# Kernel tuning notes

Hardware: AMD Instinct MI355X
Metric: run time of the kernel (lower is better)

The kernel has to match this reference:

```python
import jax, jax.numpy as jnp
import numpy as np
from math import comb

N_DERIV = 4          # num_derivatives
ODE_DIM = 512        # ode_dimension
K = ODE_DIM * (N_DERIV + 1)


def _build_system(n, d):
    # system_matrices_1d: A_1d = flip(pascal), Q_1d = flip(hilbert), chol(Q_1d)
    x = np.arange(n + 1)
    B = np.array([[comb(i, j) for j in range(n + 1)] for i in range(n + 1)], dtype=np.float64)
    A1 = B[::-1, ::-1]                                  # flip both axes
    Hil = 1.0 / (x[:, None] + x[None, :] + 1.0)
    Q1 = Hil[::-1, ::-1]
    L1 = np.linalg.cholesky(Q1)
    a = np.kron(np.eye(d), A1)
    q = np.kron(np.eye(d), L1)
    return jnp.asarray(a, jnp.float32), jnp.asarray(q, jnp.float32)


def _qr_r(x):
    # sqrtm_to_cholesky: upper-triangular factor from reduced QR
    return jnp.linalg.qr(x)[1]


def setup_inputs() -> dict:
    key = jax.random.key(0)
    k1, k2, k3, k4, k5 = jax.random.split(key, 5)
    a, q_sqrtm_lower = _build_system(N_DERIV, ODE_DIM)
    m0 = jax.random.normal(k1, (K,), dtype=jnp.float32)
    l0 = jnp.tril(jax.random.normal(k2, (K, K), dtype=jnp.float32) * 0.05)
    H = jax.random.normal(k3, (ODE_DIM, K), dtype=jnp.float32) * 0.1
    bias = jax.random.normal(k4, (ODE_DIM,), dtype=jnp.float32)
    dt = jax.random.uniform(k5, (1,), dtype=jnp.float32, minval=0.05, maxval=0.15)
    return {"m0": m0, "l0": l0, "H": H, "bias": bias, "dt": dt,
            "a": a, "q_sqrtm_lower": q_sqrtm_lower}


def reference(m0, l0, H, bias, dt, a, q_sqrtm_lower):
    d = H.shape[0]
    k = m0.shape[0]
    n1 = k // d                       # num_derivatives + 1
    # --- assemble_preconditioner ---
    powers = jnp.arange(n1 - 1, -1, -1, dtype=m0.dtype)
    scales = jnp.exp(jax.lax.lgamma(powers + 1.0))
    pw = powers + 0.5
    adt = jnp.abs(dt[0])
    p = jnp.tile(adt ** pw / scales, d)          # (k,)
    p_inv = jnp.tile(adt ** (-pw) * scales, d)   # (k,)
    # --- extrapolate_mean ---
    m0_p = p_inv * m0
    m_ext_p = a @ m0_p
    m_ext = p * m_ext_p
    # EK-style linearized observation residual
    m_obs = H @ m_ext - bias                     # (d,)
    # --- estimate_error ---
    l_obs_ns_e = H @ (p_inv[:, None] * q_sqrtm_lower)            # (d,k)
    l_obs_raw = _qr_r(l_obs_ns_e.T).T                            # lower (d,d)
    res_white = jax.scipy.linalg.solve_triangular(l_obs_raw.T, m_obs, lower=False)
    diffusion = jnp.sqrt(jnp.dot(res_white, res_white) / res_white.size)
    error = diffusion * jnp.sqrt(jnp.einsum('nj,nj->n', l_obs_raw, l_obs_raw))
    # --- complete_extrapolation (sum_of_sqrtm_factors) ---
    R1 = (a @ (p_inv[:, None] * l0)).T           # (k,k)
    R2 = (diffusion * q_sqrtm_lower).T           # (k,k)
    l_ext_p = _qr_r(jnp.vstack([R1, R2])).T      # lower (k,k)
    l_ext = p[:, None] * l_ext_p
    # --- final_correction ---
    l_obs_ns = H @ l_ext                         # (d,k)
    l_obs = _qr_r(l_obs_ns.T).T                  # lower (d,d)
    crosscov = l_ext @ l_obs_ns.T                # (k,d)
    gain = jax.scipy.linalg.cho_solve((l_obs, True), crosscov.T).T  # (k,d)
    m_cor = m_ext - gain @ m_obs
    l_cor = l_ext - gain @ l_obs_ns
    u = jnp.reshape(m_cor, (-1, d), order='F')[0]  # derivative-0 block
    return m_cor, l_cor, u, error, diffusion
```

## Files before the change

### kernel.cpp

```cpp
#include <hip/hip_runtime.h>
#include <math.h>

#define KDIM 2560
#define DDIM 512
#define NB 64

#define QM 2560
#define QN 512
#define PW 16
#define UW 10

#define OUT_LCOR 2560
#define OUT_U    6556160
#define OUT_ERR  6556672
#define OUT_DIFF 6557184


__device__ __forceinline__ void get_pats(const float* dt, double* pp, double* pv){
  double adt = fabs((double)dt[0]);
  const double scales[5] = {24.0,6.0,2.0,1.0,1.0};
  #pragma unroll
  for (int i=0;i<5;i++){
    double pw = (double)(4-i)+0.5;
    pp[i] = pow(adt, pw)/scales[i];
    pv[i] = pow(adt,-pw)*scales[i];
  }
}

__global__ __launch_bounds__(256) void k_mext_mobs(const float* a, const float* m0, const float* H,
                                                   const float* bias, const float* dt,
                                                   double* mext, double* mobs){
  __shared__ double me[KDIM];
  __shared__ double red[256];
  double pp[5], pv[5];
  get_pats(dt, pp, pv);
  int tid=threadIdx.x;
  for (int r=tid; r<KDIM; r+=256){
    int j=r/5, i=r%5;
    const float* arow = a + (size_t)r*KDIM + 5*j;
    const float* m0b  = m0 + 5*j;
    double acc=0;
    #pragma unroll
    for (int l=0;l<5;l++) acc += (double)arow[l]*pv[l]*(double)m0b[l];
    me[r] = pp[i]*acc;
  }
  __syncthreads();
  if (blockIdx.x==0) for (int r=tid;r<KDIM;r+=256) mext[r]=me[r];
  int b = blockIdx.x;
  const float* Hr = H + (size_t)b*KDIM;
  double acc=0;
  for (int c=tid;c<KDIM;c+=256) acc += (double)Hr[c]*me[c];
  red[tid]=acc; __syncthreads();
  for (int s=128;s>0;s>>=1){ if (tid<s) red[tid]+=red[tid+s]; __syncthreads(); }
  if (tid==0) mobs[b] = red[0] - (double)bias[b];
}

__global__ void k_A(const float* H, const float* q, const float* dt, double* A){
  int idx = blockIdx.x*blockDim.x+threadIdx.x;
  if (idx >= QN*QM) return;
  double pp[5], pv[5];
  get_pats(dt, pp, pv);
  int j = idx / QM;
  int i = idx % QM;
  int bi = i/5;
  double acc=0;
  #pragma unroll
  for (int t=0;t<5;t++)
    acc += (double)H[(size_t)j*QM + 5*bi+t]*pv[t]*(double)q[(size_t)(5*bi+t)*QM + i];
  A[idx] = acc;
}

__global__ __launch_bounds__(1024) void qr_panel(double* A, double* vhead, int col0, double* Tbuf){
  __shared__ double vbuf[QM];
  __shared__ double red[1024];
  __shared__ double sh[2];
  __shared__ double VtVs[PW][PW];
  __shared__ double betas_s[PW];
  __shared__ double Tsh[PW][PW];
  int tid = threadIdx.x;
  int wid = tid >> 6, lane = tid & 63;
  for (int j=0;j<PW;j++){
    int c = col0 + j;
    double acc = 0;
    for (int r = c + tid; r < QM; r += 1024){
      double v = A[(size_t)c*QM + r];
      vbuf[r-c] = v;
      acc += v*v;
    }
    red[tid] = acc; __syncthreads();
    for (int s=512; s>0; s>>=1){ if (tid<s) red[tid]+=red[tid+s]; __syncthreads(); }
    if (tid==0){
      double s0 = red[0];
      double x1 = vbuf[0];
      double nrm = sqrt(s0);
      double alpha = (x1 >= 0.0) ? -nrm : nrm;
      double v1 = x1 - alpha;
      double vtv = s0 - 2.0*alpha*x1 + alpha*alpha;
      double b = (vtv > 0.0) ? 2.0/vtv : 0.0;
      vbuf[0] = v1;
      sh[0] = b;
      A[(size_t)c*QM + c] = alpha;
      betas_s[j] = b;
      vhead[c] = v1;
    }
    __syncthreads();
    double b = sh[0];
    int jj = j + 1 + wid;
    if (jj < PW && b != 0.0){
      int cc = col0 + jj;
      double d = 0;
      for (int r = c + lane; r < QM; r += 64)
        d += vbuf[r-c]*A[(size_t)cc*QM + r];
      #pragma unroll
      for (int off=32; off>0; off>>=1) d += __shfl_down(d, off);
      d = __shfl(d, 0);
      double sc = b*d;
      for (int r = c + lane; r < QM; r += 64)
        A[(size_t)cc*QM + r] -= sc*vbuf[r-c];
    }
    if (wid < j){
      int i = wid;
      double d = 0;
      for (int r = c + lane; r < QM; r += 64)
        d += vbuf[r-c]*A[(size_t)(col0+i)*QM + r];
      #pragma unroll
      for (int off=32; off>0; off>>=1) d += __shfl_down(d, off);
      if (lane==0) VtVs[i][j] = d;
    }
    __syncthreads();
  }
  if (tid==0){
    for (int j=0;j<PW;j++){
      double bj = betas_s[j];
      Tsh[j][j] = bj;
      for (int i=0;i<j;i++){
        double z=0;
        for (int t=i;t<j;t++) z += Tsh[i][t]*VtVs[t][j];
        Tsh[i][j] = -bj*z;
      }
    }
  }
  __syncthreads();
  for (int e=tid;e<PW*PW;e+=1024){
    int i=e/PW, j2=e%PW;
    Tbuf[e] = (j2>=i)? Tsh[i][j2] : 0.0;
  }
}

__global__ __launch_bounds__(256) void qr_update(double* A, const double* vhead,
                                                 const double* Tbuf, int col0){
  __shared__ double redu[4][PW];
  __shared__ double ysh[PW];
  __shared__ double wsh[PW];
  int tid=threadIdx.x, wid=tid>>6, lane=tid&63;
  int cc=col0+PW+blockIdx.x;
  int m=QM-col0;
  double a[UW];
  #pragma unroll
  for (int w=0;w<UW;w++){
    int lr=tid+w*256;
    a[w]=(lr<m)? A[(size_t)cc*QM+col0+lr] : 0.0;
  }
  double acc[PW];
  #pragma unroll
  for (int j=0;j<PW;j++) acc[j]=0;
  #pragma unroll
  for (int w=0;w<UW;w++){
    int lr=tid+w*256;
    if (lr<m){
      #pragma unroll
      for (int j=0;j<PW;j++){
        double vj;
        if (lr>j)       vj=A[(size_t)(col0+j)*QM+col0+lr];
        else if (lr==j) vj=vhead[col0+j];
        else            vj=0.0;
        acc[j]+=vj*a[w];
      }
    }
  }
  #pragma unroll
  for (int j=0;j<PW;j++){
    double d=acc[j];
    #pragma unroll
    for (int o=32;o>0;o>>=1) d+=__shfl_down(d,o);
    if (lane==0) redu[wid][j]=d;
  }
  __syncthreads();
  if (tid<PW){
    double y=0;
    #pragma unroll
    for (int t=0;t<4;t++) y+=redu[t][tid];
    ysh[tid]=y;
  }
  __syncthreads();
  if (tid<PW){
    double s=0;
    for (int t=0;t<=tid;t++) s+=Tbuf[t*PW+tid]*ysh[t];
    wsh[tid]=s;
  }
  __syncthreads();
  #pragma unroll
  for (int w=0;w<UW;w++){
    int lr=tid+w*256;
    if (lr<m){
      double s=0;
      #pragma unroll
      for (int j=0;j<PW;j++){
        double vj;
        if (lr>j)       vj=A[(size_t)(col0+j)*QM+col0+lr];
        else if (lr==j) vj=vhead[col0+j];
        else            vj=0.0;
        s+=vj*wsh[j];
      }
      A[(size_t)cc*QM+col0+lr]=a[w]-s;
    }
  }
}

__global__ __launch_bounds__(512) void k_rpost(const double* Aq, const double* mobs,
                                               double* scal, float* out){
  __shared__ double b[DDIM];
  __shared__ double xs[DDIM];
  __shared__ double D[NB][NB+1];
  __shared__ double red[DDIM];
  __shared__ double g1sh[DDIM];
  int tid=threadIdx.x;
  {
    double s=0;
    for (int r=0;r<=tid;r++){ double v=Aq[(size_t)tid*QM + r]; s+=v*v; }
    g1sh[tid]=s;
  }
  b[tid]=mobs[tid];
  __syncthreads();
  for (int p=7;p>=0;p--){
    int b0=p*NB;
    for (int e=tid;e<NB*NB;e+=512){ int i=e&63, j2=e>>6; D[i][j2]=Aq[(size_t)(b0+j2)*QM + b0+i]; }
    __syncthreads();
    if (tid<64){
      double bi=b[b0+tid];
      for (int k=NB-1;k>=0;k--){
        double bk=__shfl(bi,k);
        double xk=bk/D[k][k];
        if (tid<k) bi-=D[tid][k]*xk;
        if (tid==k) bi=xk;
      }
      xs[b0+tid]=bi;
    }
    __syncthreads();
    if (tid<b0){
      double s=0;
      #pragma unroll 8
      for (int j2=0;j2<NB;j2++) s+=Aq[(size_t)(b0+j2)*QM + tid]*xs[b0+j2];
      b[tid]-=s;
    }
    __syncthreads();
  }
  red[tid]=xs[tid]*xs[tid]; __syncthreads();
  for (int s=256;s>0;s>>=1){ if (tid<s) red[tid]+=red[tid+s]; __syncthreads(); }
  double diff=sqrt(red[0]/(double)DDIM);
  if (tid==0){ scal[10]=diff; out[OUT_DIFF]=(float)diff; }
  out[OUT_ERR+tid]=(float)(diff*sqrt(fmax(g1sh[tid],0.0)));
}

__global__ void k_X(const float* a, const float* l0, const float* dt, float* X){
  int idx=blockIdx.x*blockDim.x+threadIdx.x;
  if (idx>=KDIM*KDIM) return;
  double pp[5], pv[5];
  get_pats(dt, pp, pv);
  int r=idx/KDIM, c=idx%KDIM;
  int j=r/5;
  const float* arow = a + (size_t)r*KDIM + 5*j;
  double acc=0;
  #pragma unroll
  for (int l=0;l<5;l++)
    acc += (double)arow[l]*pv[l]*(double)l0[(size_t)(5*j+l)*KDIM+c];
  X[idx]=(float)acc;
}

template<typename TA,int ATR,typename TB,int BTR,int MODE>
__global__ __launch_bounds__(256) void gemm64(const TA* __restrict__ A,int lda,
                                              const TB* __restrict__ B,int ldb,
                                              void* __restrict__ Cv,int ldc,
                                              int K,int kmode){
  __shared__ double As[16][65];
  __shared__ double Bs[16][65];
  int tid=threadIdx.x, tx=tid&15, ty=tid>>4;
  int n0=blockIdx.x*64, m0=blockIdx.y*64;
  int ks=0, ke=K;
  if (kmode==1) ks=n0;
  else if (kmode==2) ke=min(K,n0+64);
  else if (kmode==3) ke=min(K,m0+64);
  else if (kmode==4) ks=m0;
  double acc[4][4]={};
  for (int k0=ks;k0<ke;k0+=16){
    if (ATR){
      for (int e=tid;e<16*64;e+=256){int k=e>>6,mm=e&63; As[k][mm]=(double)A[(size_t)(k0+k)*lda+m0+mm];}
    } else {
      for (int e=tid;e<64*16;e+=256){int mm=e>>4,k=e&15; As[k][mm]=(double)A[(size_t)(m0+mm)*lda+k0+k];}
    }
    if (BTR){
      for (int e=tid;e<64*16;e+=256){int nn=e>>4,k=e&15; Bs[k][nn]=(double)B[(size_t)(n0+nn)*ldb+k0+k];}
    } else {
      for (int e=tid;e<16*64;e+=256){int k=e>>6,nn=e&63; Bs[k][nn]=(double)B[(size_t)(k0+k)*ldb+n0+nn];}
    }
    __syncthreads();
    #pragma unroll
    for (int t=0;t<16;t++){
      double av[4],bv[4];
      #pragma unroll
      for (int i=0;i<4;i++){av[i]=As[t][ty+16*i];bv[i]=Bs[t][tx+16*i];}
      #pragma unroll
      for (int i=0;i<4;i++)
        #pragma unroll
        for (int j=0;j<4;j++) acc[i][j]+=av[i]*bv[j];
    }
    __syncthreads();
  }
  #pragma unroll
  for (int i=0;i<4;i++){
    #pragma unroll
    for (int j=0;j<4;j++){
      size_t idx=(size_t)(m0+ty+16*i)*ldc+n0+tx+16*j;
      if (MODE==0) ((double*)Cv)[idx]=acc[i][j];
      else if (MODE==1) ((double*)Cv)[idx]-=acc[i][j];
      else ((float*)Cv)[idx]=(float)acc[i][j];
    }
  }
}

__global__ __launch_bounds__(256) void syrk_lower(const float* __restrict__ X, const float* __restrict__ q,
                                                  const double* __restrict__ scal,
                                                  double* __restrict__ G, int n){
  int S0=blockIdx.x*64, R0=blockIdx.y*64;
  if (S0>R0) return;
  __shared__ double As[16][65];
  __shared__ double Bs[16][65];
  int tid=threadIdx.x, tx=tid&15, ty=tid>>4;
  int kend=min(n, S0+80);
  double acc[4][4]={};
  for (int k0=0;k0<kend;k0+=16){
    for (int e=tid;e<64*16;e+=256){int mm=e>>4,k=e&15; As[k][mm]=(double)X[(size_t)(R0+mm)*n+k0+k];}
    for (int e=tid;e<64*16;e+=256){int nn=e>>4,k=e&15; Bs[k][nn]=(double)X[(size_t)(S0+nn)*n+k0+k];}
    __syncthreads();
    #pragma unroll
    for (int t=0;t<16;t++){
      double av[4],bv[4];
      #pragma unroll
      for (int i=0;i<4;i++){av[i]=As[t][ty+16*i];bv[i]=Bs[t][tx+16*i];}
      #pragma unroll
      for (int i=0;i<4;i++)
        #pragma unroll
        for (int j=0;j<4;j++) acc[i][j]+=av[i]*bv[j];
    }
    __syncthreads();
  }
  double dd = scal[10]*scal[10];
  #pragma unroll
  for (int i=0;i<4;i++)
    #pragma unroll
    for (int j=0;j<4;j++){
      int r=R0+ty+16*i, c=S0+tx+16*j;
      double v=acc[i][j];
      if (c<=r && (r/5)==(c/5)){
        double qq=0;
        #pragma unroll
        for (int k=0;k<5;k++) qq += (double)q[(size_t)(r%5)*KDIM+k]*(double)q[(size_t)(c%5)*KDIM+k];
        v += dd*qq;
      }
      G[(size_t)r*n+c]=v;
    }
}

__global__ __launch_bounds__(256) void chol_diag(double* A, int n, int k0){
  __shared__ double P[NB][NB+1];
  int tid=threadIdx.x;
  for (int e=tid;e<NB*NB;e+=256){int r=e>>6,c=e&63;P[r][c]=A[(size_t)(k0+r)*n+k0+c];}
  int tx=tid&15, ty=tid>>4;
  __syncthreads();
  for (int j=0;j<NB;j++){
    double pj=P[j][j];
    __syncthreads();
    double rpj=1.0/sqrt(fmax(pj,1e-280));
    if (tid>j && tid<NB) P[tid][j]*=rpj;
    if (tid==j) P[j][j]=sqrt(fmax(pj,1e-280));
    __syncthreads();
    #pragma unroll
    for (int a2=0;a2<4;a2++){
      int r=ty+16*a2;
      double lrj=P[r][j];
      #pragma unroll
      for (int b2=0;b2<4;b2++){
        int c=tx+16*b2;
        if (r>j && c>j && c<=r) P[r][c]-=lrj*P[c][j];
      }
    }
    __syncthreads();
  }
  for (int e=tid;e<NB*NB;e+=256){int r=e>>6,c=e&63;A[(size_t)(k0+r)*n+k0+c]=P[r][c];}
}

__global__ __launch_bounds__(256) void chol_trsm(double* A,int n,int k0){
  __shared__ double Ls[NB][NB+1];
  __shared__ double St[NB][NB+1];
  __shared__ double rec[NB];
  int tid=threadIdx.x;
  for (int e=tid;e<NB*NB;e+=256){int r=e>>6,c=e&63;Ls[r][c]=A[(size_t)(k0+r)*n+k0+c];}
  __syncthreads();
  if (tid<NB) rec[tid]=1.0/Ls[tid][tid];
  int base=k0+NB+blockIdx.x*256;
  int myrow=base+tid;
  int mychunk=tid>>6, lrow=tid&63;
  double ar[NB];
  for (int ch=0;ch<4;ch++){
    int r0=base+ch*64;
    for (int e=tid;e<NB*NB;e+=256){
      int r=e>>6,c=e&63;
      if (r0+r<n) St[r][c]=A[(size_t)(r0+r)*n+k0+c];
    }
    __syncthreads();
    if (mychunk==ch && myrow<n){
      #pragma unroll
      for (int c=0;c<NB;c++) ar[c]=St[lrow][c];
    }
    __syncthreads();
  }
  if (myrow<n){
    #pragma unroll
    for (int j=0;j<NB;j++){
      double s=ar[j];
      #pragma unroll
      for (int t=0;t<j;t++) s-=ar[t]*Ls[j][t];
      ar[j]=s*rec[j];
    }
  }
  for (int ch=0;ch<4;ch++){
    int r0=base+ch*64;
    if (mychunk==ch && myrow<n){
      #pragma unroll
      for (int c=0;c<NB;c++) St[lrow][c]=ar[c];
    }
    __syncthreads();
    for (int e=tid;e<NB*NB;e+=256){
      int r=e>>6,c=e&63;
      if (r0+r<n) A[(size_t)(r0+r)*n+k0+c]=St[r][c];
    }
    __syncthreads();
  }
}

__global__ __launch_bounds__(256) void chol_syrk_fd(double* A,int n,int k0){
  int ts0=k0+NB;
  int S0=ts0+blockIdx.x*64, R0=ts0+blockIdx.y*64;
  if (S0>R0) return;
  __shared__ double As[16][65];
  __shared__ double Bs[16][65];
  __shared__ double P[NB][NB+1];
  int tid=threadIdx.x, tx=tid&15, ty=tid>>4;
  double acc[4][4]={};
  for (int k0i=0;k0i<NB;k0i+=16){
    for (int e=tid;e<64*16;e+=256){int mm=e>>4,k=e&15; As[k][mm]=A[(size_t)(R0+mm)*n+k0+k0i+k];}
    for (int e=tid;e<64*16;e+=256){int nn=e>>4,k=e&15; Bs[k][nn]=A[(size_t)(S0+nn)*n+k0+k0i+k];}
    __syncthreads();
    #pragma unroll
    for (int t=0;t<16;t++){
      double av[4],bv[4];
      #pragma unroll
      for (int i=0;i<4;i++){av[i]=As[t][ty+16*i];bv[i]=Bs[t][tx+16*i];}
      #pragma unroll
      for (int i=0;i<4;i++)
        #pragma unroll
        for (int j=0;j<4;j++) acc[i][j]+=av[i]*bv[j];
    }
    __syncthreads();
  }
  if (!(blockIdx.x==0 && blockIdx.y==0)){
    #pragma unroll
    for (int i=0;i<4;i++)
      #pragma unroll
      for (int j=0;j<4;j++)
        A[(size_t)(R0+ty+16*i)*n+S0+tx+16*j]-=acc[i][j];
    return;
  }
  #pragma unroll
  for (int i=0;i<4;i++)
    #pragma unroll
    for (int j=0;j<4;j++)
      P[ty+16*i][tx+16*j] = A[(size_t)(R0+ty+16*i)*n+S0+tx+16*j] - acc[i][j];
  __syncthreads();
  for (int j=0;j<NB;j++){
    double pj=P[j][j];
    __syncthreads();
    double rpj=1.0/sqrt(fmax(pj,1e-280));
    if (tid>j && tid<NB) P[tid][j]*=rpj;
    if (tid==j) P[j][j]=sqrt(fmax(pj,1e-280));
    __syncthreads();
    #pragma unroll
    for (int a2=0;a2<4;a2++){
      int r=ty+16*a2;
      double lrj=P[r][j];
      #pragma unroll
      for (int b2=0;b2<4;b2++){
        int c=tx+16*b2;
        if (r>j && c>j && c<=r) P[r][c]-=lrj*P[c][j];
      }
    }
    __syncthreads();
  }
  for (int e=tid;e<NB*NB;e+=256){int r=e>>6,c=e&63;A[(size_t)(ts0+r)*n+ts0+c]=P[r][c];}
}

__global__ void k_extract(const double* G2, const float* dt, float* lext){
  int idx=blockIdx.x*blockDim.x+threadIdx.x;
  if (idx>=KDIM*KDIM) return;
  double pp[5], pv[5];
  get_pats(dt, pp, pv);
  int r=idx/KDIM, c=idx%KDIM;
  double v = (c<=r)? pp[r%5]*G2[idx] : 0.0;
  lext[idx]=(float)v;
}

__global__ __launch_bounds__(256) void trinv_diag(const double* S, double* Linv){
  __shared__ double Ls[NB][NB+1];
  __shared__ double Ti[NB][NB+1];
  int jb=blockIdx.x, tid=threadIdx.x;
  for (int e=tid; e<DDIM*NB; e+=256){
    int r=e/NB, c=e%NB;
    Linv[(size_t)r*DDIM + jb*NB + c]=0.0;
  }
  for (int e=tid;e<NB*NB;e+=256){int r=e>>6,c=e&63; Ls[r][c]=S[(size_t)(jb*NB+r)*DDIM + jb*NB+c];}
  __syncthreads();
  if (tid<NB){
    int c=tid;
    for (int r=c;r<NB;r++){
      double s=(r==c)?1.0:0.0;
      for (int t=c;t<r;t++) s-=Ls[r][t]*Ti[t][c];
      Ti[r][c]=s/Ls[r][r];
    }
    for (int r=0;r<c;r++) Ti[r][c]=0.0;
  }
  __syncthreads();
  for (int e=tid;e<NB*NB;e+=256){int r=e>>6,c=e&63; Linv[(size_t)(jb*NB+r)*DDIM + jb*NB+c]=Ti[r][c];}
}

__global__ __launch_bounds__(256) void trinv_step(const double* S, double* Linv, int d){
  __shared__ double As[16][65];
  __shared__ double Bs[16][65];
  __shared__ double Ps[NB][NB+1];
  int jb=blockIdx.x, ib=jb+d;
  int tid=threadIdx.x, tx=tid&15, ty=tid>>4;
  double acc[4][4]={};
  int kstart=jb*NB, kend=ib*NB;
  for (int k0=kstart;k0<kend;k0+=16){
    for (int e=tid;e<64*16;e+=256){int mm=e>>4,k=e&15; As[k][mm]=S[(size_t)(ib*NB+mm)*DDIM + k0+k];}
    for (int e=tid;e<16*64;e+=256){int k=e>>6,nn=e&63; Bs[k][nn]=Linv[(size_t)(k0+k)*DDIM + jb*NB+nn];}
    __syncthreads();
    #pragma unroll
    for (int t=0;t<16;t++){
      double av[4],bv[4];
      #pragma unroll
      for (int i=0;i<4;i++){av[i]=As[t][ty+16*i];bv[i]=Bs[t][tx+16*i];}
      #pragma unroll
      for (int i=0;i<4;i++)
        #pragma unroll
        for (int j=0;j<4;j++) acc[i][j]+=av[i]*bv[j];
    }
    __syncthreads();
  }
  #pragma unroll
  for (int i=0;i<4;i++)
    #pragma unroll
    for (int j=0;j<4;j++) Ps[ty+16*i][tx+16*j]=acc[i][j];
  double o[4][4]={};
  __syncthreads();
  for (int k0=0;k0<NB;k0+=16){
    for (int e=tid;e<64*16;e+=256){int mm=e>>4,k=e&15; As[k][mm]=Linv[(size_t)(ib*NB+mm)*DDIM + ib*NB+k0+k];}
    __syncthreads();
    #pragma unroll
    for (int t=0;t<16;t++){
      double av[4],bv[4];
      #pragma unroll
      for (int i=0;i<4;i++){av[i]=As[t][ty+16*i];bv[i]=Ps[k0+t][tx+16*i];}
      #pragma unroll
      for (int i=0;i<4;i++)
        #pragma unroll
        for (int j=0;j<4;j++) o[i][j]+=av[i]*bv[j];
    }
    __syncthreads();
  }
  #pragma unroll
  for (int i=0;i<4;i++)
    #pragma unroll
    for (int j=0;j<4;j++)
      Linv[(size_t)(ib*NB+ty+16*i)*DDIM + jb*NB+tx+16*j] = -o[i][j];
}

__global__ void k_mcor(const double* Z, const double* mobs, const double* mext, float* out){
  __shared__ double mo[DDIM];
  for (int s=threadIdx.x;s<DDIM;s+=256) mo[s]=mobs[s];
  __syncthreads();
  int r=blockIdx.x*256+threadIdx.x;
  if (r>=KDIM) return;
  double acc=0;
  for (int s=0;s<DDIM;s++) acc += Z[(size_t)s*KDIM+r]*mo[s];
  double mc = mext[r]-acc;
  out[r]=(float)mc;
  if (r%5==0) out[OUT_U + r/5]=(float)mc;
}

__global__ __launch_bounds__(256) void k_lcor(const double* __restrict__ Z, const float* __restrict__ lobs,
                                              const float* __restrict__ lext, float* __restrict__ out){
  __shared__ double As[16][65];
  __shared__ double Bs[16][65];
  int tid=threadIdx.x, tx=tid&15, ty=tid>>4;
  int n0=blockIdx.x*64, m0=blockIdx.y*64;
  double acc[4][4]={};
  for (int k0=0;k0<DDIM;k0+=16){
    for (int e=tid;e<16*64;e+=256){int k=e>>6,mm=e&63; As[k][mm]=Z[(size_t)(k0+k)*KDIM+m0+mm];}
    for (int e=tid;e<16*64;e+=256){int k=e>>6,nn=e&63; Bs[k][nn]=(double)lobs[(size_t)(k0+k)*KDIM+n0+nn];}
    __syncthreads();
    #pragma unroll
    for (int t=0;t<16;t++){
      double av[4],bv[4];
      #pragma unroll
      for (int i=0;i<4;i++){av[i]=As[t][ty+16*i];bv[i]=Bs[t][tx+16*i];}
      #pragma unroll
      for (int i=0;i<4;i++)
        #pragma unroll
        for (int j=0;j<4;j++) acc[i][j]+=av[i]*bv[j];
    }
    __syncthreads();
  }
  #pragma unroll
  for (int i=0;i<4;i++)
    #pragma unroll
    for (int j=0;j<4;j++){
      size_t idx=(size_t)(m0+ty+16*i)*KDIM+n0+tx+16*j;
      out[OUT_LCOR+idx]=(float)((double)lext[idx]-acc[i][j]);
    }
}

extern "C" void kernel_launch(void* const* d_in, const int* in_sizes, int n_in,
                              void* d_out, int out_size, void* d_ws, size_t ws_size,
                              hipStream_t stream) {
  const float* m0  = (const float*)d_in[0];
  const float* l0  = (const float*)d_in[1];
  const float* H   = (const float*)d_in[2];
  const float* bias= (const float*)d_in[3];
  const float* dt  = (const float*)d_in[4];
  const float* a   = (const float*)d_in[5];
  const float* q   = (const float*)d_in[6];
  float* out = (float*)d_out;

  char* w=(char*)d_ws;
  auto alloc=[&](size_t bytes)->char*{ char* p=w; w += ((bytes+255)/256)*256; return p; };
  double* scal  =(double*)alloc(16*8);
  double* mext  =(double*)alloc((size_t)KDIM*8);
  double* mobs  =(double*)alloc((size_t)DDIM*8);
  double* vheadA=(double*)alloc((size_t)QN*8);
  double* Tbuf  =(double*)alloc((size_t)PW*PW*8);
  double* Aq    =(double*)alloc((size_t)QM*QN*8);
  double* S     =(double*)alloc((size_t)DDIM*DDIM*8);
  double* G2    =(double*)alloc((size_t)KDIM*KDIM*8);
  float*  LOBS  =(float*) alloc((size_t)DDIM*KDIM*4);
  float*  X     =(float*) alloc((size_t)KDIM*KDIM*4);
  float*  LEXT  = X;
  double* Linv  = G2;
  double* C2    = Linv + (size_t)DDIM*DDIM;
  double* Y     = C2   + (size_t)DDIM*KDIM;
  double* Z     = Y    + (size_t)DDIM*KDIM;

  k_mext_mobs<<<DDIM,256,0,stream>>>(a, m0, H, bias, dt, mext, mobs);

  k_A<<<(QN*QM+255)/256,256,0,stream>>>(H, q, dt, Aq);
  for (int p=0;p<QN/PW;p++){
    int col0=p*PW;
    qr_panel<<<1,1024,0,stream>>>(Aq, vheadA, col0, Tbuf);
    int ntr = QN - col0 - PW;
    if (ntr>0) qr_update<<<ntr,256,0,stream>>>(Aq, vheadA, Tbuf, col0);
  }
  k_rpost<<<1,512,0,stream>>>(Aq, mobs, scal, out);

  k_X<<<(KDIM*KDIM+255)/256,256,0,stream>>>(a, l0, dt, X);
  syrk_lower<<<dim3(KDIM/64,KDIM/64),256,0,stream>>>(X, q, scal, G2, KDIM);
  chol_diag<<<1,256,0,stream>>>(G2, KDIM, 0);
  for (int k0=0;k0+NB<KDIM;k0+=NB){
    int m = KDIM-k0-NB;
    chol_trsm<<<(m+255)/256,256,0,stream>>>(G2, KDIM, k0);
    chol_syrk_fd<<<dim3(m/64,m/64),256,0,stream>>>(G2, KDIM, k0);
  }
  k_extract<<<(KDIM*KDIM+255)/256,256,0,stream>>>(G2, dt, LEXT);

  gemm64<float,0,float,0,2><<<dim3(KDIM/64,DDIM/64),256,0,stream>>>(H,KDIM, LEXT,KDIM, LOBS,KDIM, KDIM, 1);
  gemm64<float,0,float,1,0><<<dim3(DDIM/64,DDIM/64),256,0,stream>>>(LOBS,KDIM, LOBS,KDIM, S,DDIM, KDIM, 0);
  chol_diag<<<1,256,0,stream>>>(S, DDIM, 0);
  for (int k0=0;k0+NB<DDIM;k0+=NB){
    int m = DDIM-k0-NB;
    chol_trsm<<<(m+255)/256,256,0,stream>>>(S, DDIM, k0);
    chol_syrk_fd<<<dim3(m/64,m/64),256,0,stream>>>(S, DDIM, k0);
  }
  trinv_diag<<<8,256,0,stream>>>(S, Linv);
  for (int d=1;d<8;d++)
    trinv_step<<<8-d,256,0,stream>>>(S, Linv, d);
  gemm64<float,0,float,1,0><<<dim3(KDIM/64,DDIM/64),256,0,stream>>>(LOBS,KDIM, LEXT,KDIM, C2,KDIM, KDIM, 2);
  gemm64<double,0,double,0,0><<<dim3(KDIM/64,DDIM/64),256,0,stream>>>(Linv,DDIM, C2,KDIM, Y,KDIM, DDIM, 3);
  gemm64<double,1,double,0,0><<<dim3(KDIM/64,DDIM/64),256,0,stream>>>(Linv,DDIM, Y,KDIM, Z,KDIM, DDIM, 4);

  k_mcor<<<(KDIM+255)/256,256,0,stream>>>(Z, mobs, mext, out);
  k_lcor<<<dim3(KDIM/64,KDIM/64),256,0,stream>>>(Z, LOBS, LEXT, out);
}
```

Before: 17.14 ms.

## Compress tall QR by Cholesky of bottom Gram block before Householder

The 2560x512 tall QR used for the observation Cholesky is shrunk: the bottom 2048 rows are replaced by the Cholesky factor of their Gram matrix (computed with gemm plus blocked Cholesky), so Householder QR runs on a 1024x512 stack. The panel kernel is rewritten to keep the panel columns in registers with warp-shuffle reductions instead of shared-memory tree reductions, and the dt-derived scale factors are computed once in a setup kernel instead of with pow calls in every thread. This cuts the memory traffic and serial panel work of the 32-step QR, at the cost of extra launches and forming a Gram matrix, which squares the conditioning of that block.

```diff
diff --git a/kernel.cpp b/kernel.cpp
--- a/kernel.cpp
+++ b/kernel.cpp
@@ -6,9 +6,10 @@
 #define NB 64
 
 #define QM 2560
+#define QM2 1024
 #define QN 512
 #define PW 16
-#define UW 10
+#define UW 4
 
 #define OUT_LCOR 2560
 #define OUT_U    6556160
@@ -16,24 +17,26 @@
 #define OUT_DIFF 6557184
 
 
-__device__ __forceinline__ void get_pats(const float* dt, double* pp, double* pv){
-  double adt = fabs((double)dt[0]);
-  const double scales[5] = {24.0,6.0,2.0,1.0,1.0};
-  #pragma unroll
-  for (int i=0;i<5;i++){
-    double pw = (double)(4-i)+0.5;
-    pp[i] = pow(adt, pw)/scales[i];
-    pv[i] = pow(adt,-pw)*scales[i];
+__global__ void k_setup(const float* dt, double* scal){
+  if (threadIdx.x==0 && blockIdx.x==0){
+    double adt = fabs((double)dt[0]);
+    const double scales[5] = {24.0,6.0,2.0,1.0,1.0};
+    for (int i=0;i<5;i++){
+      double pw = (double)(4-i)+0.5;
+      scal[i]   = pow(adt, pw)/scales[i];
+      scal[5+i] = pow(adt,-pw)*scales[i];
+    }
   }
 }
 
 __global__ __launch_bounds__(256) void k_mext_mobs(const float* a, const float* m0, const float* H,
-                                                   const float* bias, const float* dt,
+                                                   const float* bias, const double* scal,
                                                    double* mext, double* mobs){
   __shared__ double me[KDIM];
   __shared__ double red[256];
   double pp[5], pv[5];
-  get_pats(dt, pp, pv);
+  #pragma unroll
+  for (int i=0;i<5;i++){ pp[i]=scal[i]; pv[i]=scal[5+i]; }
   int tid=threadIdx.x;
   for (int r=tid; r<KDIM; r+=256){
     int j=r/5, i=r%5;
@@ -55,11 +58,13 @@
   if (tid==0) mobs[b] = red[0] - (double)bias[b];
 }
 
-__global__ void k_A(const float* H, const float* q, const float* dt, double* A){
+__global__ void k_A2(const float* H, const float* q, const double* scal,
+                     double* Atop, double* Abot){
   int idx = blockIdx.x*blockDim.x+threadIdx.x;
   if (idx >= QN*QM) return;
-  double pp[5], pv[5];
-  get_pats(dt, pp, pv);
+  double pv[5];
+  #pragma unroll
+  for (int t=0;t<5;t++) pv[t]=scal[5+t];
   int j = idx / QM;
   int i = idx % QM;
   int bi = i/5;
@@ -67,83 +72,97 @@
   #pragma unroll
   for (int t=0;t<5;t++)
     acc += (double)H[(size_t)j*QM + 5*bi+t]*pv[t]*(double)q[(size_t)(5*bi+t)*QM + i];
-  A[idx] = acc;
+  if (i < 512) Atop[(size_t)j*QM2 + i] = acc;
+  else         Abot[(size_t)j*2048 + (i-512)] = acc;
+}
+
+__global__ void k_copyB(const double* Gbot, double* AQ){
+  int idx = blockIdx.x*blockDim.x+threadIdx.x;
+  if (idx >= 512*512) return;
+  int c = idx/512, rr = idx%512;
+  AQ[(size_t)c*QM2 + 512 + rr] = (rr<=c) ? Gbot[(size_t)c*512 + rr] : 0.0;
 }
 
 __global__ __launch_bounds__(1024) void qr_panel(double* A, double* vhead, int col0, double* Tbuf){
-  __shared__ double vbuf[QM];
-  __shared__ double red[1024];
-  __shared__ double sh[2];
+  __shared__ double redw[16][PW];
+  __shared__ double rednorm[16];
+  __shared__ double sh[3];
+  __shared__ double wsh[PW];
+  __shared__ double alphas[PW], betas[PW];
   __shared__ double VtVs[PW][PW];
-  __shared__ double betas_s[PW];
   __shared__ double Tsh[PW][PW];
-  int tid = threadIdx.x;
-  int wid = tid >> 6, lane = tid & 63;
+  int tid=threadIdx.x, wid=tid>>6, lane=tid&63;
+  int m = QM2 - col0;
+  bool on = tid < m;
+  double x[PW];
+  #pragma unroll
+  for (int j=0;j<PW;j++)
+    x[j] = on ? A[(size_t)(col0+j)*QM2 + col0 + tid] : 0.0;
   for (int j=0;j<PW;j++){
-    int c = col0 + j;
-    double acc = 0;
-    for (int r = c + tid; r < QM; r += 1024){
-      double v = A[(size_t)c*QM + r];
-      vbuf[r-c] = v;
-      acc += v*v;
-    }
-    red[tid] = acc; __syncthreads();
-    for (int s=512; s>0; s>>=1){ if (tid<s) red[tid]+=red[tid+s]; __syncthreads(); }
+    double v0 = (tid>=j && on)? x[j] : 0.0;
+    double ps = v0*v0;
+    #pragma unroll
+    for (int o=32;o>0;o>>=1) ps += __shfl_down(ps,o);
+    if (lane==0) rednorm[wid]=ps;
+    if (tid==j) sh[0]=x[j];
+    __syncthreads();
     if (tid==0){
-      double s0 = red[0];
-      double x1 = vbuf[0];
-      double nrm = sqrt(s0);
-      double alpha = (x1 >= 0.0) ? -nrm : nrm;
-      double v1 = x1 - alpha;
-      double vtv = s0 - 2.0*alpha*x1 + alpha*alpha;
-      double b = (vtv > 0.0) ? 2.0/vtv : 0.0;
-      vbuf[0] = v1;
-      sh[0] = b;
-      A[(size_t)c*QM + c] = alpha;
-      betas_s[j] = b;
-      vhead[c] = v1;
-    }
-    __syncthreads();
-    double b = sh[0];
-    int jj = j + 1 + wid;
-    if (jj < PW && b != 0.0){
-      int cc = col0 + jj;
-      double d = 0;
-      for (int r = c + lane; r < QM; r += 64)
-        d += vbuf[r-c]*A[(size_t)cc*QM + r];
-      #pragma unroll
-      for (int off=32; off>0; off>>=1) d += __shfl_down(d, off);
-      d = __shfl(d, 0);
-      double sc = b*d;
-      for (int r = c + lane; r < QM; r += 64)
-        A[(size_t)cc*QM + r] -= sc*vbuf[r-c];
-    }
-    if (wid < j){
-      int i = wid;
-      double d = 0;
-      for (int r = c + lane; r < QM; r += 64)
-        d += vbuf[r-c]*A[(size_t)(col0+i)*QM + r];
-      #pragma unroll
-      for (int off=32; off>0; off>>=1) d += __shfl_down(d, off);
-      if (lane==0) VtVs[i][j] = d;
-    }
-    __syncthreads();
-  }
-  if (tid==0){
-    for (int j=0;j<PW;j++){
-      double bj = betas_s[j];
-      Tsh[j][j] = bj;
-      for (int i=0;i<j;i++){
-        double z=0;
-        for (int t=i;t<j;t++) z += Tsh[i][t]*VtVs[t][j];
-        Tsh[i][j] = -bj*z;
-      }
+      double s0=0;
+      for (int t=0;t<16;t++) s0+=rednorm[t];
+      double x1=sh[0];
+      double nrm=sqrt(s0);
+      double alpha=(x1>=0.0)?-nrm:nrm;
+      double v1=x1-alpha;
+      double vtv=s0-2.0*alpha*x1+alpha*alpha;
+      double b=(vtv>0.0)?2.0/vtv:0.0;
+      sh[1]=v1; sh[2]=b;
+      alphas[j]=alpha; betas[j]=b;
+      vhead[col0+j]=v1;
+    }
+    __syncthreads();
+    if (tid==j) x[j]=sh[1];
+    double b=sh[2];
+    double v=(tid>=j && on)? x[j] : 0.0;
+    #pragma unroll
+    for (int t=0;t<PW;t++){
+      if (t==j) continue;
+      double p=v*x[t];
+      #pragma unroll
+      for (int o=32;o>0;o>>=1) p+=__shfl_down(p,o);
+      if (lane==0) redw[wid][t]=p;
+    }
+    __syncthreads();
+    if (tid<PW && tid!=j){
+      double tot=0;
+      #pragma unroll
+      for (int t2=0;t2<16;t2++) tot+=redw[t2][tid];
+      if (tid>j) wsh[tid]=b*tot;
+      else       VtVs[tid][j]=tot;
+    }
+    __syncthreads();
+    if (v!=0.0){
+      for (int t=j+1;t<PW;t++) x[t]-=wsh[t]*v;
+    }
+  }
+  __syncthreads();
+  if (tid<PW){
+    int i=tid;
+    Tsh[i][i]=betas[i];
+    for (int j2=i+1;j2<PW;j2++){
+      double z=0;
+      for (int t=i;t<j2;t++) z+=Tsh[i][t]*VtVs[t][j2];
+      Tsh[i][j2]=-betas[j2]*z;
     }
   }
   __syncthreads();
   for (int e=tid;e<PW*PW;e+=1024){
     int i=e/PW, j2=e%PW;
     Tbuf[e] = (j2>=i)? Tsh[i][j2] : 0.0;
+  }
+  if (on){
+    #pragma unroll
+    for (int j=0;j<PW;j++)
+      A[(size_t)(col0+j)*QM2 + col0 + tid] = (tid==j)? alphas[j] : x[j];
   }
 }
 
@@ -154,12 +173,12 @@
   __shared__ double wsh[PW];
   int tid=threadIdx.x, wid=tid>>6, lane=tid&63;
   int cc=col0+PW+blockIdx.x;
-  int m=QM-col0;
+  int m=QM2-col0;
   double a[UW];
   #pragma unroll
   for (int w=0;w<UW;w++){
     int lr=tid+w*256;
-    a[w]=(lr<m)? A[(size_t)cc*QM+col0+lr] : 0.0;
+    a[w]=(lr<m)? A[(size_t)cc*QM2+col0+lr] : 0.0;
   }
   double acc[PW];
   #pragma unroll
@@ -171,7 +190,7 @@
       #pragma unroll
       for (int j=0;j<PW;j++){
         double vj;
-        if (lr>j)       vj=A[(size_t)(col0+j)*QM+col0+lr];
+        if (lr>j)       vj=A[(size_t)(col0+j)*QM2+col0+lr];
         else if (lr==j) vj=vhead[col0+j];
         else            vj=0.0;
         acc[j]+=vj*a[w];
@@ -207,12 +226,12 @@
       #pragma unroll
       for (int j=0;j<PW;j++){
         double vj;
-        if (lr>j)       vj=A[(size_t)(col0+j)*QM+col0+lr];
+        if (lr>j)       vj=A[(size_t)(col0+j)*QM2+col0+lr];
         else if (lr==j) vj=vhead[col0+j];
         else            vj=0.0;
         s+=vj*wsh[j];
       }
-      A[(size_t)cc*QM+col0+lr]=a[w]-s;
+      A[(size_t)cc*QM2+col0+lr]=a[w]-s;
     }
   }
 }
@@ -227,14 +246,14 @@
   int tid=threadIdx.x;
   {
     double s=0;
-    for (int r=0;r<=tid;r++){ double v=Aq[(size_t)tid*QM + r]; s+=v*v; }
+    for (int r=0;r<=tid;r++){ double v=Aq[(size_t)tid*QM2 + r]; s+=v*v; }
     g1sh[tid]=s;
   }
   b[tid]=mobs[tid];
   __syncthreads();
   for (int p=7;p>=0;p--){
     int b0=p*NB;
-    for (int e=tid;e<NB*NB;e+=512){ int i=e&63, j2=e>>6; D[i][j2]=Aq[(size_t)(b0+j2)*QM + b0+i]; }
+    for (int e=tid;e<NB*NB;e+=512){ int i=e&63, j2=e>>6; D[i][j2]=Aq[(size_t)(b0+j2)*QM2 + b0+i]; }
     __syncthreads();
     if (tid<64){
       double bi=b[b0+tid];
@@ -250,7 +269,7 @@
     if (tid<b0){
       double s=0;
       #pragma unroll 8
-      for (int j2=0;j2<NB;j2++) s+=Aq[(size_t)(b0+j2)*QM + tid]*xs[b0+j2];
+      for (int j2=0;j2<NB;j2++) s+=Aq[(size_t)(b0+j2)*QM2 + tid]*xs[b0+j2];
       b[tid]-=s;
     }
     __syncthreads();
@@ -262,11 +281,12 @@
   out[OUT_ERR+tid]=(float)(diff*sqrt(fmax(g1sh[tid],0.0)));
 }
 
-__global__ void k_X(const float* a, const float* l0, const float* dt, float* X){
+__global__ void k_X(const float* a, const float* l0, const double* scal, float* X){
   int idx=blockIdx.x*blockDim.x+threadIdx.x;
   if (idx>=KDIM*KDIM) return;
-  double pp[5], pv[5];
-  get_pats(dt, pp, pv);
+  double pv[5];
+  #pragma unroll
+  for (int t=0;t<5;t++) pv[t]=scal[5+t];
   int r=idx/KDIM, c=idx%KDIM;
   int j=r/5;
   const float* arow = a + (size_t)r*KDIM + 5*j;
@@ -509,13 +529,11 @@
   for (int e=tid;e<NB*NB;e+=256){int r=e>>6,c=e&63;A[(size_t)(ts0+r)*n+ts0+c]=P[r][c];}
 }
 
-__global__ void k_extract(const double* G2, const float* dt, float* lext){
+__global__ void k_extract(const double* G2, const double* scal, float* lext){
   int idx=blockIdx.x*blockDim.x+threadIdx.x;
   if (idx>=KDIM*KDIM) return;
-  double pp[5], pv[5];
-  get_pats(dt, pp, pv);
   int r=idx/KDIM, c=idx%KDIM;
-  double v = (c<=r)? pp[r%5]*G2[idx] : 0.0;
+  double v = (c<=r)? scal[r%5]*G2[idx] : 0.0;
   lext[idx]=(float)v;
 }
 
@@ -658,29 +676,40 @@
   double* mobs  =(double*)alloc((size_t)DDIM*8);
   double* vheadA=(double*)alloc((size_t)QN*8);
   double* Tbuf  =(double*)alloc((size_t)PW*PW*8);
-  double* Aq    =(double*)alloc((size_t)QM*QN*8);
+  double* AQ    =(double*)alloc((size_t)QM2*QN*8);
   double* S     =(double*)alloc((size_t)DDIM*DDIM*8);
   double* G2    =(double*)alloc((size_t)KDIM*KDIM*8);
   float*  LOBS  =(float*) alloc((size_t)DDIM*KDIM*4);
   float*  X     =(float*) alloc((size_t)KDIM*KDIM*4);
   float*  LEXT  = X;
+  double* Abot  = G2;
+  double* Gbot  = Abot + (size_t)2048*512;
   double* Linv  = G2;
   double* C2    = Linv + (size_t)DDIM*DDIM;
   double* Y     = C2   + (size_t)DDIM*KDIM;
   double* Z     = Y    + (size_t)DDIM*KDIM;
 
-  k_mext_mobs<<<DDIM,256,0,stream>>>(a, m0, H, bias, dt, mext, mobs);
-
-  k_A<<<(QN*QM+255)/256,256,0,stream>>>(H, q, dt, Aq);
+  k_setup<<<1,1,0,stream>>>(dt, scal);
+  k_mext_mobs<<<DDIM,256,0,stream>>>(a, m0, H, bias, scal, mext, mobs);
+
+  k_A2<<<(QN*QM+255)/256,256,0,stream>>>(H, q, scal, AQ, Abot);
+  gemm64<double,0,double,1,0><<<dim3(8,8),256,0,stream>>>(Abot,2048, Abot,2048, Gbot,512, 2048, 0);
+  chol_diag<<<1,256,0,stream>>>(Gbot,512,0);
+  for (int k0=0;k0+NB<512;k0+=NB){
+    int m = 512-k0-NB;
+    chol_trsm<<<(m+255)/256,256,0,stream>>>(Gbot,512,k0);
+    chol_syrk_fd<<<dim3(m/64,m/64),256,0,stream>>>(Gbot,512,k0);
+  }
+  k_copyB<<<(512*512+255)/256,256,0,stream>>>(Gbot, AQ);
   for (int p=0;p<QN/PW;p++){
     int col0=p*PW;
-    qr_panel<<<1,1024,0,stream>>>(Aq, vheadA, col0, Tbuf);
+    qr_panel<<<1,1024,0,stream>>>(AQ, vheadA, col0, Tbuf);
     int ntr = QN - col0 - PW;
-    if (ntr>0) qr_update<<<ntr,256,0,stream>>>(Aq, vheadA, Tbuf, col0);
-  }
-  k_rpost<<<1,512,0,stream>>>(Aq, mobs, scal, out);
-
-  k_X<<<(KDIM*KDIM+255)/256,256,0,stream>>>(a, l0, dt, X);
+    if (ntr>0) qr_update<<<ntr,256,0,stream>>>(AQ, vheadA, Tbuf, col0);
+  }
+  k_rpost<<<1,512,0,stream>>>(AQ, mobs, scal, out);
+
+  k_X<<<(KDIM*KDIM+255)/256,256,0,stream>>>(a, l0, scal, X);
   syrk_lower<<<dim3(KDIM/64,KDIM/64),256,0,stream>>>(X, q, scal, G2, KDIM);
   chol_diag<<<1,256,0,stream>>>(G2, KDIM, 0);
   for (int k0=0;k0+NB<KDIM;k0+=NB){
@@ -688,7 +717,7 @@
     chol_trsm<<<(m+255)/256,256,0,stream>>>(G2, KDIM, k0);
     chol_syrk_fd<<<dim3(m/64,m/64),256,0,stream>>>(G2, KDIM, k0);
   }
-  k_extract<<<(KDIM*KDIM+255)/256,256,0,stream>>>(G2, dt, LEXT);
+  k_extract<<<(KDIM*KDIM+255)/256,256,0,stream>>>(G2, scal, LEXT);
 
   gemm64<float,0,float,0,2><<<dim3(KDIM/64,DDIM/64),256,0,stream>>>(H,KDIM, LEXT,KDIM, LOBS,KDIM, KDIM, 1);
   gemm64<float,0,float,1,0><<<dim3(DDIM/64,DDIM/64),256,0,stream>>>(LOBS,KDIM, LOBS,KDIM, S,DDIM, KDIM, 0);
```

New measurement: 15.55 ms. 1.1x faster.
